# Kernel optimization log

Measured on AMD Instinct MI355X. Metric: run time of the kernel, lower is better.

The kernel has to match this reference:

```python
import jax, jax.numpy as jnp
import numpy as np

D_MODEL = 1024
N_HEADS = 16
N_KV = 4
HEAD_DIM = D_MODEL // N_HEADS  # 64
EPS = 1e-5
THETA = 10000.0


def _rope_tables(S):
    half = HEAD_DIM // 2
    inv_freq = 1.0 / (THETA ** (jnp.arange(half, dtype=jnp.float32) / half))
    t = jnp.arange(S, dtype=jnp.float32)
    f = t[:, None] * inv_freq[None, :]  # [S, half]
    return jnp.cos(f), jnp.sin(f)


def _apply_rope(x, cos, sin):
    # x: [B, H, S, D]
    half = x.shape[-1] // 2
    x1, x2 = x[..., :half], x[..., half:]
    c = cos[None, None, :, :]
    s = sin[None, None, :, :]
    return jnp.concatenate([x1 * c - x2 * s, x1 * s + x2 * c], axis=-1)


def _rmsnorm(x, scale):
    rms = jnp.sqrt(jnp.mean(x * x, axis=-1, keepdims=True) + EPS)
    return x / rms * scale


def setup_inputs() -> dict:
    key = jax.random.key(0)
    ks = jax.random.split(key, 4)
    B, S = 2, 2048
    x = jax.random.normal(ks[0], (B, S, D_MODEL), dtype=jnp.float32)
    Wq = jax.random.normal(ks[1], (D_MODEL, D_MODEL), dtype=jnp.float32) * 0.02
    Wkv = jax.random.normal(ks[2], (D_MODEL, 2 * N_KV * HEAD_DIM), dtype=jnp.float32) * 0.02
    Wo = jax.random.normal(ks[3], (D_MODEL, D_MODEL), dtype=jnp.float32) * 0.02
    q_scale = jnp.ones((HEAD_DIM,), dtype=jnp.float32)
    k_scale = jnp.ones((HEAD_DIM,), dtype=jnp.float32)
    return {"x": x, "Wq": Wq, "Wkv": Wkv, "Wo": Wo,
            "q_scale": q_scale, "k_scale": k_scale}


def reference(x, Wq, Wkv, Wo, q_scale, k_scale):
    B, S, D = x.shape
    groups = N_HEADS // N_KV  # GQA group size

    # projections
    q = (x @ Wq).reshape(B, S, N_HEADS, HEAD_DIM).transpose(0, 2, 1, 3)  # [B,H,S,d]
    kv = x @ Wkv
    k, v = jnp.split(kv, 2, axis=-1)
    k = k.reshape(B, S, N_KV, HEAD_DIM).transpose(0, 2, 1, 3)  # [B,Hkv,S,d]
    v = v.reshape(B, S, N_KV, HEAD_DIM).transpose(0, 2, 1, 3)

    # per-head QK-RMSNorm (before RoPE, as in the torch module)
    q = _rmsnorm(q, q_scale)
    k = _rmsnorm(k, k_scale)

    # RoPE
    cos, sin = _rope_tables(S)
    q = _apply_rope(q, cos, sin)
    k = _apply_rope(k, cos, sin)

    # causal GQA attention (equivalent to SDPA with enable_gqa=True)
    qg = q.reshape(B, N_KV, groups, S, HEAD_DIM)
    scale = 1.0 / np.sqrt(HEAD_DIM).astype(np.float32)
    scores = jnp.einsum('bkgsd,bktd->bkgst', qg, k) * scale  # [B,Hkv,g,S,S]
    causal = jnp.tril(jnp.ones((S, S), dtype=bool))
    scores = jnp.where(causal[None, None, None], scores, -jnp.inf)
    attn = jax.nn.softmax(scores, axis=-1)
    out = jnp.einsum('bkgst,bktd->bkgsd', attn, v)
    out = out.reshape(B, N_HEADS, S, HEAD_DIM).transpose(0, 2, 1, 3).reshape(B, S, D)
    return out @ Wo
```

## Files before the change

kernel.cpp:

```cpp
#include <hip/hip_runtime.h>

#define S_LEN 2048
#define BATCH 2
#define DM    1024
#define NH    16
#define NKV   4
#define HD    64
#define MROWS (BATCH * S_LEN)
#define NQKV  1536

typedef __attribute__((ext_vector_type(8))) short bf16x8;
typedef __attribute__((ext_vector_type(4))) short s16x4;
typedef __attribute__((ext_vector_type(4))) float f32x4;

__device__ __forceinline__ unsigned short f2bf(float f) {
  unsigned int u = __float_as_uint(f);
  u += 0x7FFF + ((u >> 16) & 1);
  return (unsigned short)(u >> 16);
}

__device__ __forceinline__ void gload_lds16(const unsigned short* g, unsigned short* l) {
  __builtin_amdgcn_global_load_lds((const __attribute__((address_space(1))) void*)g,
                                   (__attribute__((address_space(3))) void*)l, 16, 0, 0);
}

__global__ __launch_bounds__(256) void cvt_x_kernel(const float* __restrict__ x,
                                                    unsigned short* __restrict__ xb, int n) {
  int i = (blockIdx.x * 256 + threadIdx.x) * 4;
  if (i < n) {
    float4 v = *reinterpret_cast<const float4*>(x + i);
    xb[i + 0] = f2bf(v.x);
    xb[i + 1] = f2bf(v.y);
    xb[i + 2] = f2bf(v.z);
    xb[i + 3] = f2bf(v.w);
  }
}

__global__ __launch_bounds__(256) void transpose_all_kernel(const float* __restrict__ Wq,
                                                            const float* __restrict__ Wkv,
                                                            const float* __restrict__ Wo,
                                                            unsigned short* __restrict__ wt1,
                                                            unsigned short* __restrict__ wot) {
  __shared__ float tile[64][65];
  int bid = blockIdx.x;
  const float* in;
  unsigned short* out;
  int R, C, bx, by;
  if (bid < 256) { in = Wq; out = wt1; R = 1024; C = 1024; bx = bid & 15; by = bid >> 4; }
  else if (bid < 384) { int k = bid - 256; in = Wkv; out = wt1 + 1024 * 1024; R = 1024; C = 512; bx = k & 7; by = k >> 3; }
  else { int k = bid - 384; in = Wo; out = wot; R = 1024; C = 1024; bx = k & 15; by = k >> 4; }
  int r0 = by * 64, c0 = bx * 64;
  int t = threadIdx.x;
  int rl = t >> 2, cs = (t & 3) * 16;
#pragma unroll
  for (int k = 0; k < 4; ++k) {
    float4 v = *reinterpret_cast<const float4*>(in + (size_t)(r0 + rl) * C + c0 + cs + 4 * k);
    tile[rl][cs + 4 * k + 0] = v.x;
    tile[rl][cs + 4 * k + 1] = v.y;
    tile[rl][cs + 4 * k + 2] = v.z;
    tile[rl][cs + 4 * k + 3] = v.w;
  }
  __syncthreads();
  int cl = t >> 2, rs = (t & 3) * 16;
  bf16x8 v0, v1;
#pragma unroll
  for (int i = 0; i < 8; ++i) v0[i] = (short)f2bf(tile[rs + i][cl]);
#pragma unroll
  for (int i = 0; i < 8; ++i) v1[i] = (short)f2bf(tile[rs + 8 + i][cl]);
  unsigned short* dst = out + (size_t)(c0 + cl) * R + r0 + rs;
  *reinterpret_cast<bf16x8*>(dst) = v0;
  *reinterpret_cast<bf16x8*>(dst + 8) = v1;
}

__global__ __launch_bounds__(256) void gemm1_fused(const unsigned short* __restrict__ A,
                                                   const unsigned short* __restrict__ BT,
                                                   const float* __restrict__ q_scale,
                                                   const float* __restrict__ k_scale,
                                                   unsigned short* __restrict__ qb,
                                                   unsigned short* __restrict__ kbuf,
                                                   unsigned short* __restrict__ vrow,
                                                   int K) {
  __shared__ __align__(16) unsigned short As[128 * 64];
  __shared__ __align__(16) unsigned short Bs[64 * 64];
  int bx = blockIdx.x;
  int row0 = blockIdx.y * 128, col0 = bx * 64;
  int t = threadIdx.x;
  int w = t >> 6, lane = t & 63, quad = lane >> 4, l16 = lane & 15;
  int srow = lane >> 3;
  int scol = (lane & 7) * 8;

  f32x4 acc[2][4];
#pragma unroll
  for (int i = 0; i < 2; ++i)
#pragma unroll
    for (int j = 0; j < 4; ++j) acc[i][j] = (f32x4){0.f, 0.f, 0.f, 0.f};

  for (int k0 = 0; k0 < K; k0 += 64) {
#pragma unroll
    for (int j = 0; j < 4; ++j)
      gload_lds16(A + (size_t)(row0 + w * 32 + j * 8 + srow) * K + k0 + scol,
                  &As[(w * 32 + j * 8) * 64]);
#pragma unroll
    for (int j = 0; j < 2; ++j)
      gload_lds16(BT + (size_t)(col0 + w * 16 + j * 8 + srow) * K + k0 + scol,
                  &Bs[(w * 16 + j * 8) * 64]);
    __syncthreads();
#pragma unroll
    for (int ks = 0; ks < 2; ++ks) {
      bf16x8 af[2], bfr[4];
#pragma unroll
      for (int i = 0; i < 2; ++i)
        af[i] = *reinterpret_cast<const bf16x8*>(&As[(w * 32 + i * 16 + l16) * 64 + ks * 32 + quad * 8]);
#pragma unroll
      for (int j = 0; j < 4; ++j)
        bfr[j] = *reinterpret_cast<const bf16x8*>(&Bs[(j * 16 + l16) * 64 + ks * 32 + quad * 8]);
#pragma unroll
      for (int i = 0; i < 2; ++i)
#pragma unroll
        for (int j = 0; j < 4; ++j)
          acc[i][j] = __builtin_amdgcn_mfma_f32_16x16x32_bf16(af[i], bfr[j], acc[i][j], 0, 0, 0);
    }
    __syncthreads();
  }

  if (bx < 20) {
    const float* scale = (bx < 16) ? q_scale : k_scale;
    float post = (bx < 16) ? 1.0f : 0.125f * 1.44269504088896f;
    float sc0 = scale[l16], sc1 = scale[16 + l16], sc2 = scale[32 + l16], sc3 = scale[48 + l16];
    float invf0 = exp2f((float)l16 * (-13.2877123795495f / 32.0f));
    float invf1 = exp2f((float)(l16 + 16) * (-13.2877123795495f / 32.0f));
#pragma unroll
    for (int i = 0; i < 2; ++i)
#pragma unroll
      for (int rg = 0; rg < 4; ++rg) {
        int row = row0 + w * 32 + i * 16 + quad * 4 + rg;
        int b = row >> 11, s = row & 2047;
        float v0 = acc[i][0][rg], v1 = acc[i][1][rg], v2 = acc[i][2][rg], v3 = acc[i][3][rg];
        float ss = v0 * v0 + v1 * v1 + v2 * v2 + v3 * v3;
        ss += __shfl_xor(ss, 1, 64);
        ss += __shfl_xor(ss, 2, 64);
        ss += __shfl_xor(ss, 4, 64);
        ss += __shfl_xor(ss, 8, 64);
        float inv_rms = 1.0f / sqrtf(ss * (1.0f / 64.0f) + 1e-5f);
        float n0 = v0 * inv_rms * sc0, n1 = v1 * inv_rms * sc1;
        float n2 = v2 * inv_rms * sc2, n3 = v3 * inv_rms * sc3;
        float f0 = (float)s * invf0, f1 = (float)s * invf1;
        float c0 = cosf(f0), s0 = sinf(f0), c1 = cosf(f1), s1 = sinf(f1);
        float o0 = (n0 * c0 - n2 * s0) * post;
        float o1 = (n1 * c1 - n3 * s1) * post;
        float o2 = (n0 * s0 + n2 * c0) * post;
        float o3 = (n1 * s1 + n3 * c1) * post;
        unsigned short* dst = (bx < 16)
            ? qb + ((size_t)(b * NH + bx) * S_LEN + s) * HD
            : kbuf + ((size_t)(b * NKV + (bx - 16)) * S_LEN + s) * HD;
        dst[l16] = f2bf(o0);
        dst[16 + l16] = f2bf(o1);
        dst[32 + l16] = f2bf(o2);
        dst[48 + l16] = f2bf(o3);
      }
  } else {
    int kvh = bx - 20;
#pragma unroll
    for (int i = 0; i < 2; ++i)
#pragma unroll
      for (int rg = 0; rg < 4; ++rg) {
        int row = row0 + w * 32 + i * 16 + quad * 4 + rg;
        unsigned short* dst = vrow + (size_t)row * 256 + kvh * 64;
        dst[l16] = f2bf(acc[i][0][rg]);
        dst[16 + l16] = f2bf(acc[i][1][rg]);
        dst[32 + l16] = f2bf(acc[i][2][rg]);
        dst[48 + l16] = f2bf(acc[i][3][rg]);
      }
  }
}

__global__ __launch_bounds__(256) void v_transpose_bf16(const unsigned short* __restrict__ vrow,
                                                        unsigned short* __restrict__ vt) {
  __shared__ unsigned short tile[64][72];
  int bkv = blockIdx.x >> 5;
  int b = bkv >> 2, kvh = bkv & 3;
  int s0 = (blockIdx.x & 31) * 64;
  int t = threadIdx.x;
  int sl = t >> 2, part = (t & 3) * 16;
  const unsigned short* src = vrow + (size_t)(b * S_LEN + s0 + sl) * 256 + kvh * 64 + part;
  *reinterpret_cast<bf16x8*>(&tile[sl][part]) = *reinterpret_cast<const bf16x8*>(src);
  *reinterpret_cast<bf16x8*>(&tile[sl][part + 8]) = *reinterpret_cast<const bf16x8*>(src + 8);
  __syncthreads();
  int d = t >> 2, sc = (t & 3) * 16;
  bf16x8 a0, a1;
#pragma unroll
  for (int i = 0; i < 8; ++i) a0[i] = (short)tile[sc + i][d];
#pragma unroll
  for (int i = 0; i < 8; ++i) a1[i] = (short)tile[sc + 8 + i][d];
  unsigned short* dst = vt + ((size_t)bkv * 64 + d) * S_LEN + s0 + sc;
  *reinterpret_cast<bf16x8*>(dst) = a0;
  *reinterpret_cast<bf16x8*>(dst + 8) = a1;
}

__global__ __launch_bounds__(256, 1) void attn_kernel(const unsigned short* __restrict__ qb,
                                                      const unsigned short* __restrict__ kbuf,
                                                      const unsigned short* __restrict__ vt,
                                                      unsigned short* __restrict__ ctx) {
  __shared__ __align__(16) unsigned short PT[4][2][16][72];
  int g = blockIdx.x >> 3;
  int bkv = blockIdx.x & 7;
  int t32 = (g < 32) ? (63 - g) : (g - 32);
  int b = bkv >> 2, kvh = bkv & 3;
  int w = threadIdx.x >> 6;
  int h = kvh * 4 + w;
  int lane = threadIdx.x & 63;
  int quad = lane >> 4, l16 = lane & 15;
  int qa = t32 * 32 + l16;
  const unsigned short* Q = qb + (size_t)(b * NH + h) * S_LEN * HD;
  const unsigned short* Kh = kbuf + (size_t)(b * NKV + kvh) * S_LEN * HD;
  const unsigned short* Vh = vt + (size_t)(b * NKV + kvh) * HD * S_LEN;

  bf16x8 bqa0 = *reinterpret_cast<const bf16x8*>(Q + (size_t)qa * HD + quad * 8);
  bf16x8 bqa1 = *reinterpret_cast<const bf16x8*>(Q + (size_t)qa * HD + 32 + quad * 8);
  bf16x8 bqb0 = *reinterpret_cast<const bf16x8*>(Q + (size_t)(qa + 16) * HD + quad * 8);
  bf16x8 bqb1 = *reinterpret_cast<const bf16x8*>(Q + (size_t)(qa + 16) * HD + 32 + quad * 8);

  bf16x8 ones;
#pragma unroll
  for (int i = 0; i < 8; ++i) ones[i] = (short)0x3F80;

  f32x4 ot[2][4];
#pragma unroll
  for (int gq = 0; gq < 2; ++gq)
#pragma unroll
    for (int i = 0; i < 4; ++i) ot[gq][i] = (f32x4){0.f, 0.f, 0.f, 0.f};
  f32x4 ol[2] = {(f32x4){0.f, 0.f, 0.f, 0.f}, (f32x4){0.f, 0.f, 0.f, 0.f}};

  int nkb = (t32 >> 1) + 1;

  bf16x8 kc0[4], kc1[4], vc0[4], vc1[4];
#pragma unroll
  for (int km = 0; km < 4; ++km) {
    const unsigned short* kp = Kh + (size_t)(km * 16 + l16) * HD;
    kc0[km] = *reinterpret_cast<const bf16x8*>(kp + quad * 8);
    kc1[km] = *reinterpret_cast<const bf16x8*>(kp + 32 + quad * 8);
    const unsigned short* vp = Vh + (size_t)(km * 16 + l16) * S_LEN;
    vc0[km] = *reinterpret_cast<const bf16x8*>(vp + quad * 8);
    vc1[km] = *reinterpret_cast<const bf16x8*>(vp + 32 + quad * 8);
  }

  for (int kbi = 0; kbi < nkb; ++kbi) {
    bool last = (kbi == nkb - 1);
    int kbase = kbi << 6;
    bf16x8 kn0[4], kn1[4], vn0[4], vn1[4];
    if (!last) {
      const unsigned short* kp = Kh + (size_t)(kbase + 64 + l16) * HD;
      const unsigned short* vp = Vh + (size_t)l16 * S_LEN + kbase + 64;
#pragma unroll
      for (int km = 0; km < 4; ++km) {
        kn0[km] = *reinterpret_cast<const bf16x8*>(kp + (size_t)(km * 16) * HD + quad * 8);
        kn1[km] = *reinterpret_cast<const bf16x8*>(kp + (size_t)(km * 16) * HD + 32 + quad * 8);
        vn0[km] = *reinterpret_cast<const bf16x8*>(vp + (size_t)(km * 16) * S_LEN + quad * 8);
        vn1[km] = *reinterpret_cast<const bf16x8*>(vp + (size_t)(km * 16) * S_LEN + 32 + quad * 8);
      }
    }
    f32x4 sa[4], sb[4];
#pragma unroll
    for (int km = 0; km < 4; ++km) {
      f32x4 s = {0.f, 0.f, 0.f, 0.f};
      s = __builtin_amdgcn_mfma_f32_16x16x32_bf16(kc0[km], bqa0, s, 0, 0, 0);
      s = __builtin_amdgcn_mfma_f32_16x16x32_bf16(kc1[km], bqa1, s, 0, 0, 0);
      sa[km] = s;
      f32x4 s2 = {0.f, 0.f, 0.f, 0.f};
      s2 = __builtin_amdgcn_mfma_f32_16x16x32_bf16(kc0[km], bqb0, s2, 0, 0, 0);
      s2 = __builtin_amdgcn_mfma_f32_16x16x32_bf16(kc1[km], bqb1, s2, 0, 0, 0);
      sb[km] = s2;
    }
    if (last) {
#pragma unroll
      for (int km = 0; km < 4; ++km)
#pragma unroll
        for (int rg = 0; rg < 4; ++rg) {
          int key = kbase + km * 16 + quad * 4 + rg;
          if (key > qa) sa[km][rg] = -1e30f;
          if (key > qa + 16) sb[km][rg] = -1e30f;
        }
    }
#pragma unroll
    for (int km = 0; km < 4; ++km) {
      float a0 = exp2f(sa[km][0]), a1 = exp2f(sa[km][1]);
      float a2 = exp2f(sa[km][2]), a3 = exp2f(sa[km][3]);
      uint2 pw;
      pw.x = __builtin_amdgcn_perm(__float_as_uint(a1), __float_as_uint(a0), 0x07060302);
      pw.y = __builtin_amdgcn_perm(__float_as_uint(a3), __float_as_uint(a2), 0x07060302);
      *reinterpret_cast<uint2*>(&PT[w][0][l16][km * 16 + quad * 4]) = pw;
      float b0 = exp2f(sb[km][0]), b1 = exp2f(sb[km][1]);
      float b2 = exp2f(sb[km][2]), b3 = exp2f(sb[km][3]);
      uint2 qw;
      qw.x = __builtin_amdgcn_perm(__float_as_uint(b1), __float_as_uint(b0), 0x07060302);
      qw.y = __builtin_amdgcn_perm(__float_as_uint(b3), __float_as_uint(b2), 0x07060302);
      *reinterpret_cast<uint2*>(&PT[w][1][l16][km * 16 + quad * 4]) = qw;
    }
    bf16x8 pa0 = *reinterpret_cast<const bf16x8*>(&PT[w][0][l16][quad * 8]);
    bf16x8 pa1 = *reinterpret_cast<const bf16x8*>(&PT[w][0][l16][32 + quad * 8]);
    bf16x8 pb0 = *reinterpret_cast<const bf16x8*>(&PT[w][1][l16][quad * 8]);
    bf16x8 pb1 = *reinterpret_cast<const bf16x8*>(&PT[w][1][l16][32 + quad * 8]);
    ol[0] = __builtin_amdgcn_mfma_f32_16x16x32_bf16(ones, pa0, ol[0], 0, 0, 0);
    ol[0] = __builtin_amdgcn_mfma_f32_16x16x32_bf16(ones, pa1, ol[0], 0, 0, 0);
    ol[1] = __builtin_amdgcn_mfma_f32_16x16x32_bf16(ones, pb0, ol[1], 0, 0, 0);
    ol[1] = __builtin_amdgcn_mfma_f32_16x16x32_bf16(ones, pb1, ol[1], 0, 0, 0);
#pragma unroll
    for (int dm = 0; dm < 4; ++dm) {
      ot[0][dm] = __builtin_amdgcn_mfma_f32_16x16x32_bf16(vc0[dm], pa0, ot[0][dm], 0, 0, 0);
      ot[0][dm] = __builtin_amdgcn_mfma_f32_16x16x32_bf16(vc1[dm], pa1, ot[0][dm], 0, 0, 0);
      ot[1][dm] = __builtin_amdgcn_mfma_f32_16x16x32_bf16(vc0[dm], pb0, ot[1][dm], 0, 0, 0);
      ot[1][dm] = __builtin_amdgcn_mfma_f32_16x16x32_bf16(vc1[dm], pb1, ot[1][dm], 0, 0, 0);
    }
    if (!last) {
#pragma unroll
      for (int km = 0; km < 4; ++km) {
        kc0[km] = kn0[km]; kc1[km] = kn1[km];
        vc0[km] = vn0[km]; vc1[km] = vn1[km];
      }
    }
  }

#pragma unroll
  for (int gq = 0; gq < 2; ++gq) {
    float inv_l = 1.0f / ol[gq][0];
    size_t base = ((size_t)(b * S_LEN) + qa + gq * 16) * DM + h * HD;
#pragma unroll
    for (int dm = 0; dm < 4; ++dm) {
      s16x4 pv;
#pragma unroll
      for (int rg = 0; rg < 4; ++rg) pv[rg] = (short)f2bf(ot[gq][dm][rg] * inv_l);
      *reinterpret_cast<s16x4*>(ctx + base + dm * 16 + quad * 4) = pv;
    }
  }
}

__global__ __launch_bounds__(256) void gemm_bt_n64(const unsigned short* __restrict__ A,
                                                   const unsigned short* __restrict__ BT,
                                                   float* __restrict__ C,
                                                   int M, int N, int K) {
  __shared__ __align__(16) unsigned short As[128 * 64];
  __shared__ __align__(16) unsigned short Bs[64 * 64];
  int row0 = blockIdx.y * 128, col0 = blockIdx.x * 64;
  int t = threadIdx.x;
  int w = t >> 6, lane = t & 63, quad = lane >> 4, l16 = lane & 15;
  int srow = lane >> 3;
  int scol = (lane & 7) * 8;

  f32x4 acc[2][4];
#pragma unroll
  for (int i = 0; i < 2; ++i)
#pragma unroll
    for (int j = 0; j < 4; ++j) acc[i][j] = (f32x4){0.f, 0.f, 0.f, 0.f};

  for (int k0 = 0; k0 < K; k0 += 64) {
#pragma unroll
    for (int j = 0; j < 4; ++j)
      gload_lds16(A + (size_t)(row0 + w * 32 + j * 8 + srow) * K + k0 + scol,
                  &As[(w * 32 + j * 8) * 64]);
#pragma unroll
    for (int j = 0; j < 2; ++j)
      gload_lds16(BT + (size_t)(col0 + w * 16 + j * 8 + srow) * K + k0 + scol,
                  &Bs[(w * 16 + j * 8) * 64]);
    __syncthreads();
#pragma unroll
    for (int ks = 0; ks < 2; ++ks) {
      bf16x8 af[2], bfr[4];
#pragma unroll
      for (int i = 0; i < 2; ++i)
        af[i] = *reinterpret_cast<const bf16x8*>(&As[(w * 32 + i * 16 + l16) * 64 + ks * 32 + quad * 8]);
#pragma unroll
      for (int j = 0; j < 4; ++j)
        bfr[j] = *reinterpret_cast<const bf16x8*>(&Bs[(j * 16 + l16) * 64 + ks * 32 + quad * 8]);
#pragma unroll
      for (int i = 0; i < 2; ++i)
#pragma unroll
        for (int j = 0; j < 4; ++j)
          acc[i][j] = __builtin_amdgcn_mfma_f32_16x16x32_bf16(af[i], bfr[j], acc[i][j], 0, 0, 0);
    }
    __syncthreads();
  }
#pragma unroll
  for (int i = 0; i < 2; ++i)
#pragma unroll
    for (int j = 0; j < 4; ++j) {
      int row = row0 + w * 32 + i * 16 + quad * 4;
      float* Cptr = C + (size_t)row * N + col0 + j * 16 + l16;
#pragma unroll
      for (int rg = 0; rg < 4; ++rg) Cptr[(size_t)rg * N] = acc[i][j][rg];
    }
}

extern "C" void kernel_launch(void* const* d_in, const int* in_sizes, int n_in,
                              void* d_out, int out_size, void* d_ws, size_t ws_size,
                              hipStream_t stream) {
  const float* x = (const float*)d_in[0];
  const float* Wq = (const float*)d_in[1];
  const float* Wkv = (const float*)d_in[2];
  const float* Wo = (const float*)d_in[3];
  const float* q_scale = (const float*)d_in[4];
  const float* k_scale = (const float*)d_in[5];
  float* out = (float*)d_out;

  char* ws = (char*)d_ws;
  size_t off = 0;
  auto alloc = [&](size_t bytes) {
    void* p = ws + off;
    off += (bytes + 255) & ~(size_t)255;
    return p;
  };
  unsigned short* xb = (unsigned short*)alloc((size_t)MROWS * DM * 2);
  unsigned short* wt1 = (unsigned short*)alloc((size_t)NQKV * DM * 2);
  unsigned short* wot = (unsigned short*)alloc((size_t)DM * DM * 2);
  unsigned short* qb = (unsigned short*)alloc((size_t)BATCH * NH * S_LEN * HD * 2);
  unsigned short* kbuf = (unsigned short*)alloc((size_t)BATCH * NKV * S_LEN * HD * 2);
  unsigned short* vrow = (unsigned short*)alloc((size_t)MROWS * NKV * HD * 2);
  unsigned short* vt = (unsigned short*)alloc((size_t)BATCH * NKV * HD * S_LEN * 2);
  unsigned short* ctx = (unsigned short*)alloc((size_t)MROWS * DM * 2);

  cvt_x_kernel<<<(MROWS * DM) / 1024, 256, 0, stream>>>(x, xb, MROWS * DM);
  transpose_all_kernel<<<640, 256, 0, stream>>>(Wq, Wkv, Wo, wt1, wot);

  gemm1_fused<<<dim3(NQKV / 64, MROWS / 128), 256, 0, stream>>>(xb, wt1, q_scale, k_scale,
                                                                qb, kbuf, vrow, DM);
  v_transpose_bf16<<<256, 256, 0, stream>>>(vrow, vt);

  attn_kernel<<<BATCH * NKV * (S_LEN / 32), 256, 0, stream>>>(qb, kbuf, vt, ctx);

  gemm_bt_n64<<<dim3(DM / 64, MROWS / 128), 256, 0, stream>>>(ctx, wot, out, MROWS, DM, DM);
}
```

Measured before the change: 198.7 us.

## Stage K/V tiles through double-buffered LDS shared across the GQA head warps

The attention kernel used to have each of the four warps (one per query head in a KV group) load the full K and V tiles from global memory into registers. Now the block loads each 64-key K/V tile once into double-buffered LDS with direct global-to-LDS 4-byte loads, and each warp reads its MFMA operands from LDS. This removes the fourfold redundant global loads and frees registers, so launch bounds are raised to allow two blocks per CU. In exchange it adds a block-wide barrier per key block and uses small 4-byte async loads, which could leave latency exposed.

Result: faster. 190.6 us (-4.1%).

```diff
diff --git a/kernel.cpp b/kernel.cpp
--- a/kernel.cpp
+++ b/kernel.cpp
@@ -22,6 +22,10 @@
 __device__ __forceinline__ void gload_lds16(const unsigned short* g, unsigned short* l) {
   __builtin_amdgcn_global_load_lds((const __attribute__((address_space(1))) void*)g,
                                    (__attribute__((address_space(3))) void*)l, 16, 0, 0);
+}
+__device__ __forceinline__ void gload_lds4(const unsigned short* g, unsigned short* l) {
+  __builtin_amdgcn_global_load_lds((const __attribute__((address_space(1))) void*)g,
+                                   (__attribute__((address_space(3))) void*)l, 4, 0, 0);
 }
 
 __global__ __launch_bounds__(256) void cvt_x_kernel(const float* __restrict__ x,
@@ -197,10 +201,14 @@
   *reinterpret_cast<bf16x8*>(dst + 8) = a1;
 }
 
-__global__ __launch_bounds__(256, 1) void attn_kernel(const unsigned short* __restrict__ qb,
+#define CH 136
+#define TILE_SH (32 * CH)
+__global__ __launch_bounds__(256, 2) void attn_kernel(const unsigned short* __restrict__ qb,
                                                       const unsigned short* __restrict__ kbuf,
                                                       const unsigned short* __restrict__ vt,
                                                       unsigned short* __restrict__ ctx) {
+  __shared__ __align__(16) unsigned short Ks[2][TILE_SH];
+  __shared__ __align__(16) unsigned short Vs[2][TILE_SH];
   __shared__ __align__(16) unsigned short PT[4][2][16][72];
   int g = blockIdx.x >> 3;
   int bkv = blockIdx.x & 7;
@@ -233,42 +241,42 @@
 
   int nkb = (t32 >> 1) + 1;
 
-  bf16x8 kc0[4], kc1[4], vc0[4], vc1[4];
-#pragma unroll
-  for (int km = 0; km < 4; ++km) {
-    const unsigned short* kp = Kh + (size_t)(km * 16 + l16) * HD;
-    kc0[km] = *reinterpret_cast<const bf16x8*>(kp + quad * 8);
-    kc1[km] = *reinterpret_cast<const bf16x8*>(kp + 32 + quad * 8);
-    const unsigned short* vp = Vh + (size_t)(km * 16 + l16) * S_LEN;
-    vc0[km] = *reinterpret_cast<const bf16x8*>(vp + quad * 8);
-    vc1[km] = *reinterpret_cast<const bf16x8*>(vp + 32 + quad * 8);
-  }
+  auto stage = [&](int kbase, int dbuf) {
+    const unsigned short* kg = Kh + (size_t)(kbase + w * 16) * HD + lane * 2;
+    const unsigned short* vg = Vh + (size_t)(w * 16 + (lane >> 5)) * S_LEN + kbase + (lane & 31) * 2;
+    unsigned short* kl = &Ks[dbuf][(w * 8) * CH];
+    unsigned short* vl = &Vs[dbuf][(w * 8) * CH];
+#pragma unroll
+    for (int c = 0; c < 8; ++c) {
+      gload_lds4(kg + (size_t)(2 * c) * HD, kl + c * CH);
+      gload_lds4(vg + (size_t)(2 * c) * S_LEN, vl + c * CH);
+    }
+  };
+
+  stage(0, 0);
+  __syncthreads();
 
   for (int kbi = 0; kbi < nkb; ++kbi) {
     bool last = (kbi == nkb - 1);
     int kbase = kbi << 6;
-    bf16x8 kn0[4], kn1[4], vn0[4], vn1[4];
-    if (!last) {
-      const unsigned short* kp = Kh + (size_t)(kbase + 64 + l16) * HD;
-      const unsigned short* vp = Vh + (size_t)l16 * S_LEN + kbase + 64;
-#pragma unroll
-      for (int km = 0; km < 4; ++km) {
-        kn0[km] = *reinterpret_cast<const bf16x8*>(kp + (size_t)(km * 16) * HD + quad * 8);
-        kn1[km] = *reinterpret_cast<const bf16x8*>(kp + (size_t)(km * 16) * HD + 32 + quad * 8);
-        vn0[km] = *reinterpret_cast<const bf16x8*>(vp + (size_t)(km * 16) * S_LEN + quad * 8);
-        vn1[km] = *reinterpret_cast<const bf16x8*>(vp + (size_t)(km * 16) * S_LEN + 32 + quad * 8);
-      }
-    }
+    if (!last) stage(kbase + 64, (kbi + 1) & 1);
+    const unsigned short* Kd = Ks[kbi & 1];
+    const unsigned short* Vd = Vs[kbi & 1];
+
     f32x4 sa[4], sb[4];
 #pragma unroll
     for (int km = 0; km < 4; ++km) {
+      int ch = km * 8 + (l16 >> 1);
+      int base = ch * CH + (l16 & 1) * 64;
+      bf16x8 k0 = *reinterpret_cast<const bf16x8*>(&Kd[base + quad * 8]);
+      bf16x8 k1 = *reinterpret_cast<const bf16x8*>(&Kd[base + 32 + quad * 8]);
       f32x4 s = {0.f, 0.f, 0.f, 0.f};
-      s = __builtin_amdgcn_mfma_f32_16x16x32_bf16(kc0[km], bqa0, s, 0, 0, 0);
-      s = __builtin_amdgcn_mfma_f32_16x16x32_bf16(kc1[km], bqa1, s, 0, 0, 0);
+      s = __builtin_amdgcn_mfma_f32_16x16x32_bf16(k0, bqa0, s, 0, 0, 0);
+      s = __builtin_amdgcn_mfma_f32_16x16x32_bf16(k1, bqa1, s, 0, 0, 0);
       sa[km] = s;
       f32x4 s2 = {0.f, 0.f, 0.f, 0.f};
-      s2 = __builtin_amdgcn_mfma_f32_16x16x32_bf16(kc0[km], bqb0, s2, 0, 0, 0);
-      s2 = __builtin_amdgcn_mfma_f32_16x16x32_bf16(kc1[km], bqb1, s2, 0, 0, 0);
+      s2 = __builtin_amdgcn_mfma_f32_16x16x32_bf16(k0, bqb0, s2, 0, 0, 0);
+      s2 = __builtin_amdgcn_mfma_f32_16x16x32_bf16(k1, bqb1, s2, 0, 0, 0);
       sb[km] = s2;
     }
     if (last) {
@@ -306,18 +314,16 @@
     ol[1] = __builtin_amdgcn_mfma_f32_16x16x32_bf16(ones, pb1, ol[1], 0, 0, 0);
 #pragma unroll
     for (int dm = 0; dm < 4; ++dm) {
-      ot[0][dm] = __builtin_amdgcn_mfma_f32_16x16x32_bf16(vc0[dm], pa0, ot[0][dm], 0, 0, 0);
-      ot[0][dm] = __builtin_amdgcn_mfma_f32_16x16x32_bf16(vc1[dm], pa1, ot[0][dm], 0, 0, 0);
-      ot[1][dm] = __builtin_amdgcn_mfma_f32_16x16x32_bf16(vc0[dm], pb0, ot[1][dm], 0, 0, 0);
-      ot[1][dm] = __builtin_amdgcn_mfma_f32_16x16x32_bf16(vc1[dm], pb1, ot[1][dm], 0, 0, 0);
-    }
-    if (!last) {
-#pragma unroll
-      for (int km = 0; km < 4; ++km) {
-        kc0[km] = kn0[km]; kc1[km] = kn1[km];
-        vc0[km] = vn0[km]; vc1[km] = vn1[km];
-      }
-    }
+      int ch = dm * 8 + (l16 >> 1);
+      int base = ch * CH + (l16 & 1) * 64;
+      bf16x8 v0 = *reinterpret_cast<const bf16x8*>(&Vd[base + quad * 8]);
+      bf16x8 v1 = *reinterpret_cast<const bf16x8*>(&Vd[base + 32 + quad * 8]);
+      ot[0][dm] = __builtin_amdgcn_mfma_f32_16x16x32_bf16(v0, pa0, ot[0][dm], 0, 0, 0);
+      ot[0][dm] = __builtin_amdgcn_mfma_f32_16x16x32_bf16(v1, pa1, ot[0][dm], 0, 0, 0);
+      ot[1][dm] = __builtin_amdgcn_mfma_f32_16x16x32_bf16(v0, pb0, ot[1][dm], 0, 0, 0);
+      ot[1][dm] = __builtin_amdgcn_mfma_f32_16x16x32_bf16(v1, pb1, ot[1][dm], 0, 0, 0);
+    }
+    __syncthreads();
   }
 
 #pragma unroll
```
